# Optimization experiments

Measured on AMD Instinct MI355X. Metric: run time of the kernel, lower is better.

## Reference

```python
import jax, jax.numpy as jnp
import numpy as np

DIM = 384
HEADS = 8
SR = 2
BN_EPS = 1e-5


def setup_inputs() -> dict:
    key = jax.random.key(0)
    ks = jax.random.split(key, 8)
    B, Hh, Ww = 4, 64, 64
    N = Hh * Ww
    Nk = (Hh // SR) * (Ww // SR)
    w = lambda k, s: jax.random.normal(k, s, jnp.float32) * 0.02
    return {
        "x": jax.random.normal(ks[0], (B, N, DIM), jnp.float32),
        "relative_pos": jax.random.normal(ks[1], (HEADS, N, Nk), jnp.float32) * 0.02,
        "H": Hh,
        "W": Ww,
        "Wq": w(ks[2], (DIM, DIM)),
        "Wk": w(ks[3], (DIM, DIM)),
        "Wv": w(ks[4], (DIM, DIM)),
        "Wp": w(ks[5], (DIM, DIM)),
        "bp": jnp.zeros((DIM,), jnp.float32),
        "sr_w": w(ks[6], (DIM, 1, SR, SR)),  # depthwise conv, OIHW with groups=DIM
        "sr_b": jnp.zeros((DIM,), jnp.float32),
        "bn_gamma": jnp.ones((DIM,), jnp.float32),
        "bn_beta": jnp.zeros((DIM,), jnp.float32),
        "bn_mean": jnp.zeros((DIM,), jnp.float32),
        "bn_var": jnp.ones((DIM,), jnp.float32),
    }


def reference(x, relative_pos, Wq, Wk, Wv, Wp, bp, sr_w, sr_b,
              bn_gamma, bn_beta, bn_mean, bn_var, H, W):
    B, N, C = x.shape
    hd = C // HEADS
    scale = hd ** (-0.5)
    # q projection -> [B, heads, N, hd]
    q = (x @ Wq.T).reshape(B, N, HEADS, hd).transpose(0, 2, 1, 3)
    # spatial reduction: depthwise conv stride SR + BatchNorm (eval mode)
    x_ = x.transpose(0, 2, 1).reshape(B, C, H, W)
    y = jax.lax.conv_general_dilated(
        x_, sr_w, window_strides=(SR, SR), padding="VALID",
        feature_group_count=C,
        dimension_numbers=("NCHW", "OIHW", "NCHW"))
    y = y + sr_b[None, :, None, None]
    inv = jax.lax.rsqrt(bn_var + BN_EPS) * bn_gamma
    y = (y - bn_mean[None, :, None, None]) * inv[None, :, None, None] \
        + bn_beta[None, :, None, None]
    xk = y.reshape(B, C, -1).transpose(0, 2, 1)  # [B, Nk, C]
    Nk = xk.shape[1]
    k = (xk @ Wk.T).reshape(B, Nk, HEADS, hd).transpose(0, 2, 1, 3)
    v = (xk @ Wv.T).reshape(B, Nk, HEADS, hd).transpose(0, 2, 1, 3)
    # scores with additive relative-position bias (broadcast over batch)
    attn = jnp.einsum("bhnd,bhmd->bhnm", q, k) * scale + relative_pos
    attn = jax.nn.softmax(attn, axis=-1)
    out = jnp.einsum("bhnm,bhmd->bhnd", attn, v)
    out = out.transpose(0, 2, 1, 3).reshape(B, N, C)
    return out @ Wp.T + bp
```

## Files before the change

kernel.cpp:

```cpp
#include <hip/hip_runtime.h>
#include <hip/hip_bf16.h>

#define LOG2E 1.4426950408889634f

typedef short bf16x8 __attribute__((ext_vector_type(8)));
typedef float f32x4  __attribute__((ext_vector_type(4)));

#define OFF_BPf  16
#define OFF_SRWf (OFF_BPf + 384)
#define OFF_SRBf (OFF_SRWf + 1536)
#define OFF_GAf  (OFF_SRBf + 384)
#define OFF_BEf  (OFF_GAf + 384)
#define OFF_MUf  (OFF_BEf + 384)
#define OFF_VAf  (OFF_MUf + 384)
#define U_XB 7712
#define U_WQ (U_XB + 6291456)
#define U_WK (U_WQ + 147456)
#define U_WV (U_WK + 147456)
#define U_WP (U_WV + 147456)
#define U_XK (U_WP + 147456)
#define U_QB (U_XK + 1572864)
#define U_KB (U_QB + 6291456)
#define U_VT (U_KB + 1572864)
#define U_OB (U_VT + 1572864)

static __device__ __forceinline__ float bfu(unsigned short u){ return __uint_as_float(((unsigned)u) << 16); }
static __device__ __forceinline__ float bf_lo(unsigned v){ return __uint_as_float(v << 16); }
static __device__ __forceinline__ float bf_hi(unsigned v){ return __uint_as_float(v & 0xFFFF0000u); }
static __device__ __forceinline__ unsigned short f2bf(float f){
  unsigned u = __float_as_uint(f);
  u += 0x7FFFu + ((u >> 16) & 1u);
  return (unsigned short)(u >> 16);
}
static __device__ __forceinline__ unsigned pkcvt(float a, float b){
  float2 f; f.x = a; f.y = b;
  __hip_bfloat162 h = __float22bfloat162_rn(f);
  union { __hip_bfloat162 h2; unsigned u; } cv; cv.h2 = h; return cv.u;
}
static __device__ __forceinline__ unsigned pk2bf(float a, float b){
  return pkcvt(a, b);
}
static __device__ __forceinline__ float fast_exp2(float x){ return __builtin_amdgcn_exp2f(x); }
static __device__ __forceinline__ void gld_lds16(const void* g, void* l){
  __builtin_amdgcn_global_load_lds((const __attribute__((address_space(1))) void*)g,
                                   (__attribute__((address_space(3))) void*)l, 16, 0, 0);
}

__global__ void detect_bf16(const unsigned* __restrict__ xraw, int* __restrict__ flag){
  unsigned w = xraw[threadIdx.x];
  unsigned e = (w >> 7) & 0xFFu;
  unsigned long long m = __ballot(e >= 118u && e <= 137u);
  if (threadIdx.x == 0) *flag = (__popcll(m) >= 40) ? 1 : 0;
}

static __device__ __forceinline__ void cp8_bf(unsigned short* dst, const void* src, int off, bool bf){
  if (bf) { *(uint4*)dst = *(const uint4*)((const unsigned short*)src + off); }
  else {
    const float* s = (const float*)src + off;
    float4 a = *(const float4*)s, b = *(const float4*)(s + 4);
    uint4 o; o.x = pk2bf(a.x, a.y); o.y = pk2bf(a.z, a.w);
    o.z = pk2bf(b.x, b.y); o.w = pk2bf(b.z, b.w);
    *(uint4*)dst = o;
  }
}
static __device__ __forceinline__ void cp8_f(float* dst, const void* src, int off, bool bf){
  if (bf) {
    const unsigned short* s = (const unsigned short*)src + off;
    uint4 w = *(const uint4*)s;
    float4 a, b;
    a.x = bf_lo(w.x); a.y = bf_hi(w.x); a.z = bf_lo(w.y); a.w = bf_hi(w.y);
    b.x = bf_lo(w.z); b.y = bf_hi(w.z); b.z = bf_lo(w.w); b.w = bf_hi(w.w);
    *(float4*)dst = a; *(float4*)(dst + 4) = b;
  } else {
    const float* s = (const float*)src + off;
    *(float4*)dst = *(const float4*)s;
    *(float4*)(dst + 4) = *(const float4*)(s + 4);
  }
}

__global__ __launch_bounds__(256) void convert_all(
    const void* x, const void* wq, const void* wk, const void* wv, const void* wp,
    const void* bp, const void* srw, const void* srb, const void* ga, const void* be,
    const void* mu, const void* va, float* ws){
  const bool bf = ((const int*)ws)[0] != 0;
  unsigned short* u = (unsigned short*)ws;
  int g = blockIdx.x * 256 + threadIdx.x;
  if (g < 786432) { cp8_bf(u + U_XB + g*8, x,  g*8, bf); return; }  g -= 786432;
  if (g < 18432)  { cp8_bf(u + U_WQ + g*8, wq, g*8, bf); return; }  g -= 18432;
  if (g < 18432)  { cp8_bf(u + U_WK + g*8, wk, g*8, bf); return; }  g -= 18432;
  if (g < 18432)  { cp8_bf(u + U_WV + g*8, wv, g*8, bf); return; }  g -= 18432;
  if (g < 18432)  { cp8_bf(u + U_WP + g*8, wp, g*8, bf); return; }  g -= 18432;
  if (g < 192)    { cp8_f(ws + OFF_SRWf + g*8, srw, g*8, bf); return; } g -= 192;
  if (g < 48)     { cp8_f(ws + OFF_BPf  + g*8, bp,  g*8, bf); return; } g -= 48;
  if (g < 48)     { cp8_f(ws + OFF_SRBf + g*8, srb, g*8, bf); return; } g -= 48;
  if (g < 48)     { cp8_f(ws + OFF_GAf  + g*8, ga,  g*8, bf); return; } g -= 48;
  if (g < 48)     { cp8_f(ws + OFF_BEf  + g*8, be,  g*8, bf); return; } g -= 48;
  if (g < 48)     { cp8_f(ws + OFF_MUf  + g*8, mu,  g*8, bf); return; } g -= 48;
  if (g < 48)     { cp8_f(ws + OFF_VAf  + g*8, va,  g*8, bf); }
}

__global__ __launch_bounds__(256) void sr_bn(const unsigned short* __restrict__ xb,
    const float* __restrict__ wsf, unsigned short* __restrict__ xkb){
  int idx = blockIdx.x * 256 + threadIdx.x;
  int c8 = idx % 48;
  int nk = (idx / 48) & 1023;
  int b  = idx / (48 * 1024);
  int i = nk >> 5, j = nk & 31;
  int c0 = c8 * 8;
  const unsigned short* xp = xb + ((size_t)(b*4096 + i*128 + j*2))*384 + c0;
  unsigned aw[4], bw[4], cw[4], dw[4];
  *(uint4*)aw = *(const uint4*)(xp);
  *(uint4*)bw = *(const uint4*)(xp + 384);
  *(uint4*)cw = *(const uint4*)(xp + 64*384);
  *(uint4*)dw = *(const uint4*)(xp + 65*384);
  unsigned out[4];
  #pragma unroll
  for (int k2 = 0; k2 < 4; ++k2) {
    float r2[2];
    #pragma unroll
    for (int half = 0; half < 2; ++half) {
      int k = k2*2 + half;
      int c = c0 + k;
      float xa = half ? bf_hi(aw[k2]) : bf_lo(aw[k2]);
      float xbv = half ? bf_hi(bw[k2]) : bf_lo(bw[k2]);
      float xc = half ? bf_hi(cw[k2]) : bf_lo(cw[k2]);
      float xd = half ? bf_hi(dw[k2]) : bf_lo(dw[k2]);
      float acc = xa*wsf[OFF_SRWf+c*4] + xbv*wsf[OFF_SRWf+c*4+1]
                + xc*wsf[OFF_SRWf+c*4+2] + xd*wsf[OFF_SRWf+c*4+3];
      float inv = rsqrtf(wsf[OFF_VAf+c] + 1e-5f) * wsf[OFF_GAf+c];
      r2[half] = (acc + wsf[OFF_SRBf+c] - wsf[OFF_MUf+c]) * inv + wsf[OFF_BEf+c];
    }
    out[k2] = pkcvt(r2[0], r2[1]);
  }
  *(uint4*)(xkb + (size_t)idx*8) = *(uint4*)out;
}

__global__ __launch_bounds__(256) void proj_qkv(unsigned short* __restrict__ u){
  int z, by;
  if (blockIdx.y < 128)      { z = 0; by = blockIdx.y; }
  else if (blockIdx.y < 160) { z = 1; by = blockIdx.y - 128; }
  else                       { z = 2; by = blockIdx.y - 160; }
  const unsigned short* A = u + ((z == 0) ? U_XB : U_XK);
  const unsigned short* W = u + ((z == 0) ? U_WQ : (z == 1) ? U_WK : U_WV);

  __shared__ unsigned short As[128][40];
  __shared__ unsigned short Ws[128][40];
  const int tid = threadIdx.x;
  const int wave = tid >> 6, lane = tid & 63, lg = lane >> 4, ln = lane & 15;
  const int m0 = by * 128, n0 = blockIdx.x * 128;
  const int wm = (wave >> 1) * 64, wn = (wave & 1) * 64;
  f32x4 acc[4][4];
  #pragma unroll
  for (int i = 0; i < 4; ++i)
    #pragma unroll
    for (int j = 0; j < 4; ++j) acc[i][j] = (f32x4){0.f,0.f,0.f,0.f};

  const int arow = tid >> 1, acol = (tid & 1) * 16;
  for (int kt = 0; kt < 384; kt += 32) {
    uint4 a0 = *(const uint4*)&A[(size_t)(m0+arow)*384 + kt + acol];
    uint4 a1 = *(const uint4*)&A[(size_t)(m0+arow)*384 + kt + acol + 8];
    uint4 w0 = *(const uint4*)&W[(size_t)(n0+arow)*384 + kt + acol];
    uint4 w1 = *(const uint4*)&W[(size_t)(n0+arow)*384 + kt + acol + 8];
    __syncthreads();
    *(uint4*)&As[arow][acol] = a0;  *(uint4*)&As[arow][acol+8] = a1;
    *(uint4*)&Ws[arow][acol] = w0;  *(uint4*)&Ws[arow][acol+8] = w1;
    __syncthreads();
    bf16x8 af[4], wf[4];
    #pragma unroll
    for (int mi = 0; mi < 4; ++mi) af[mi] = *(const bf16x8*)&As[wm + mi*16 + ln][lg*8];
    #pragma unroll
    for (int ni = 0; ni < 4; ++ni) wf[ni] = *(const bf16x8*)&Ws[wn + ni*16 + ln][lg*8];
    #pragma unroll
    for (int mi = 0; mi < 4; ++mi)
      #pragma unroll
      for (int ni = 0; ni < 4; ++ni)
        acc[mi][ni] = __builtin_amdgcn_mfma_f32_16x16x32_bf16(af[mi], wf[ni], acc[mi][ni], 0, 0, 0);
  }

  unsigned short* outQ = u + U_QB;
  unsigned short* outK = u + U_KB;
  unsigned short* outV = u + U_VT;
  #pragma unroll
  for (int mi = 0; mi < 4; ++mi)
    #pragma unroll
    for (int ni = 0; ni < 4; ++ni) {
      int gcol = n0 + wn + ni*16 + ln;
      if (z == 2) {
        int grow0 = m0 + wm + mi*16 + lg*4;
        int hh = gcol / 48, d = gcol - hh*48;
        int bb = grow0 >> 10, mk = grow0 & 1023;
        uint2 st; st.x = pkcvt(acc[mi][ni][0], acc[mi][ni][1]);
        st.y = pkcvt(acc[mi][ni][2], acc[mi][ni][3]);
        *(uint2*)&outV[((size_t)((bb*8 + hh)*48 + d))*1024 + mk] = st;
      } else {
        unsigned short* dst = (z == 0) ? outQ : outK;
        #pragma unroll
        for (int r = 0; r < 4; ++r) {
          int grow = m0 + wm + mi*16 + lg*4 + r;
          dst[(size_t)grow*384 + gcol] = f2bf(acc[mi][ni][r]);
        }
      }
    }
}

__global__ __launch_bounds__(256) void gemm_out(const unsigned short* __restrict__ A,
    const unsigned short* __restrict__ W, const float* __restrict__ bias,
    void* __restrict__ out, const int* __restrict__ flag){
  __shared__ unsigned short As[128][40];
  __shared__ unsigned short Ws[128][40];
  const int tid = threadIdx.x;
  const int wave = tid >> 6, lane = tid & 63, lg = lane >> 4, ln = lane & 15;
  const int m0 = blockIdx.y * 128, n0 = blockIdx.x * 128;
  const int wm = (wave >> 1) * 64, wn = (wave & 1) * 64;
  f32x4 acc[4][4];
  #pragma unroll
  for (int i = 0; i < 4; ++i)
    #pragma unroll
    for (int j = 0; j < 4; ++j) acc[i][j] = (f32x4){0.f,0.f,0.f,0.f};

  const int arow = tid >> 1, acol = (tid & 1) * 16;
  for (int kt = 0; kt < 384; kt += 32) {
    uint4 a0 = *(const uint4*)&A[(size_t)(m0+arow)*384 + kt + acol];
    uint4 a1 = *(const uint4*)&A[(size_t)(m0+arow)*384 + kt + acol + 8];
    uint4 w0 = *(const uint4*)&W[(size_t)(n0+arow)*384 + kt + acol];
    uint4 w1 = *(const uint4*)&W[(size_t)(n0+arow)*384 + kt + acol + 8];
    __syncthreads();
    *(uint4*)&As[arow][acol] = a0;  *(uint4*)&As[arow][acol+8] = a1;
    *(uint4*)&Ws[arow][acol] = w0;  *(uint4*)&Ws[arow][acol+8] = w1;
    __syncthreads();
    bf16x8 af[4], wf[4];
    #pragma unroll
    for (int mi = 0; mi < 4; ++mi) af[mi] = *(const bf16x8*)&As[wm + mi*16 + ln][lg*8];
    #pragma unroll
    for (int ni = 0; ni < 4; ++ni) wf[ni] = *(const bf16x8*)&Ws[wn + ni*16 + ln][lg*8];
    #pragma unroll
    for (int mi = 0; mi < 4; ++mi)
      #pragma unroll
      for (int ni = 0; ni < 4; ++ni)
        acc[mi][ni] = __builtin_amdgcn_mfma_f32_16x16x32_bf16(af[mi], wf[ni], acc[mi][ni], 0, 0, 0);
  }

  const bool bff = (*flag != 0);
  #pragma unroll
  for (int mi = 0; mi < 4; ++mi)
    #pragma unroll
    for (int ni = 0; ni < 4; ++ni)
      #pragma unroll
      for (int r = 0; r < 4; ++r) {
        int grow = m0 + wm + mi*16 + lg*4 + r;
        int gcol = n0 + wn + ni*16 + ln;
        float v = acc[mi][ni][r] + bias[gcol];
        if (bff) ((unsigned short*)out)[(size_t)grow*384 + gcol] = f2bf(v);
        else     ((float*)out)[(size_t)grow*384 + gcol] = v;
      }
}

__global__ __launch_bounds__(256, 4) void attn_mfma(const unsigned short* __restrict__ qb,
    const unsigned short* __restrict__ kb, const unsigned short* __restrict__ vt,
    const void* __restrict__ rel, const int* __restrict__ flag,
    unsigned short* __restrict__ ob){
  __shared__ __align__(16) unsigned short Kbuf[2][6*512];
  __shared__ __align__(16) unsigned short Vbuf[8*384];
  __shared__ __align__(16) unsigned short Ps[4][16][64];
  __shared__ float Ls[4][32];
  const int x = blockIdx.x;
  const int b = x >> 5, nb = x & 31, h = blockIdx.y;
  const int tid = threadIdx.x, wave = tid >> 6, lane = tid & 63;
  const int lg = lane >> 4, ln = lane & 15;
  const int qrow0 = nb * 128 + wave * 32;
  const bool bfm = (*flag != 0);
  const float SCL = 0.14433756729740643f * LOG2E;

  bf16x8 qf0[2], qf1[2];
  #pragma unroll
  for (int qt = 0; qt < 2; ++qt) {
    const unsigned short* qp = qb + ((size_t)(b*4096 + qrow0 + qt*16 + ln))*384 + h*48;
    qf0[qt] = *(const bf16x8*)(qp + lg*8);
    bf16x8 z = {0,0,0,0,0,0,0,0};
    if (lg < 2) z = *(const bf16x8*)(qp + 32 + lg*8);
    qf1[qt] = z;
  }

  f32x4 o[2][3];
  #pragma unroll
  for (int qt = 0; qt < 2; ++qt) { o[qt][0] = (f32x4){0.f,0.f,0.f,0.f}; o[qt][1] = o[qt][0]; o[qt][2] = o[qt][0]; }
  float lsum[2] = {0.f, 0.f};

  const float* relf = (const float*)rel;
  const unsigned short* relh = (const unsigned short*)rel;
  const size_t rbase = ((size_t)(h*4096 + qrow0 + ln)) * 1024;
  const size_t kbase = (size_t)(b*1024) * 384 + (size_t)h*48;
  const size_t vbase = ((size_t)(b*8 + h)) * 48 * 1024;

  const unsigned swz = (unsigned)((ln & 7) << 4);
  char* psrow = (char*)&Ps[wave][ln][0];

  const int jk1 = wave;
  const int jk2 = 4 + wave;
  const int jv1 = wave;
  const int jv2 = 2 + wave;
  int s1i = jv1*64 + lane;  int c1 = s1i/48, d1 = s1i - 48*c1;
  size_t vg1 = vbase + (size_t)d1*1024 + c1*8;
  int s2i = jv2*64 + lane;  int c2 = s2i/48, d2 = s2i - 48*c2;
  size_t vg2 = vbase + (size_t)d2*1024 + c2*8;

  gld_lds16(kb + kbase + (size_t)lane*384 + jk1*8, &Kbuf[0][jk1*512]);
  if (wave < 2) gld_lds16(kb + kbase + (size_t)lane*384 + jk2*8, &Kbuf[0][jk2*512]);

  #pragma unroll 1
  for (int t = 0; t < 16; ++t) {
    const int cbuf = t & 1, nbuf = cbuf ^ 1;
    __syncthreads();

    uint2 rr[2][4];
    if (bfm) {
      #pragma unroll
      for (int qt = 0; qt < 2; ++qt)
        #pragma unroll
        for (int mt = 0; mt < 4; ++mt)
          rr[qt][mt] = *(const uint2*)(relh + rbase + (size_t)qt*16384 + t*64 + mt*16 + lg*4);
    } else {
      #pragma unroll
      for (int qt = 0; qt < 2; ++qt)
        #pragma unroll
        for (int mt = 0; mt < 4; ++mt) {
          float4 q_ = *(const float4*)(relf + rbase + (size_t)qt*16384 + t*64 + mt*16 + lg*4);
          rr[qt][mt].x = pkcvt(q_.x, q_.y); rr[qt][mt].y = pkcvt(q_.z, q_.w);
        }
    }

    gld_lds16(vt + vg1 + t*64, &Vbuf[jv1*512]);
    if (wave >= 2) gld_lds16(vt + vg2 + t*64, &Vbuf[jv2*512]);
    const int T = (t + 1 < 16) ? t + 1 : 15;
    gld_lds16(kb + kbase + (size_t)T*24576 + (size_t)lane*384 + jk1*8, &Kbuf[nbuf][jk1*512]);
    if (wave < 2) gld_lds16(kb + kbase + (size_t)T*24576 + (size_t)lane*384 + jk2*8, &Kbuf[nbuf][jk2*512]);

    f32x4 s0[4];
    #pragma unroll
    for (int mt = 0; mt < 4; ++mt) {
      bf16x8 k0 = *(const bf16x8*)&Kbuf[cbuf][lg*512 + (mt*16 + ln)*8];
      bf16x8 k1 = {0,0,0,0,0,0,0,0};
      if (lg < 2) k1 = *(const bf16x8*)&Kbuf[cbuf][(4 + lg)*512 + (mt*16 + ln)*8];
      s0[mt] = __builtin_amdgcn_mfma_f32_16x16x32_bf16(k0, qf0[0], (f32x4){0.f,0.f,0.f,0.f}, 0, 0, 0);
      s0[mt] = __builtin_amdgcn_mfma_f32_16x16x32_bf16(k1, qf1[0], s0[mt], 0, 0, 0);
    }
    {
      float lacc = 0.f;
      #pragma unroll
      for (int mt = 0; mt < 4; ++mt) {
        float r0 = bf_lo(rr[0][mt].x), r1 = bf_hi(rr[0][mt].x);
        float r2 = bf_lo(rr[0][mt].y), r3 = bf_hi(rr[0][mt].y);
        float p0 = fast_exp2(fmaf(s0[mt][0], SCL, r0 * LOG2E));
        float p1 = fast_exp2(fmaf(s0[mt][1], SCL, r1 * LOG2E));
        float p2 = fast_exp2(fmaf(s0[mt][2], SCL, r2 * LOG2E));
        float p3 = fast_exp2(fmaf(s0[mt][3], SCL, r3 * LOG2E));
        lacc += (p0 + p1) + (p2 + p3);
        uint2 w; w.x = pkcvt(p0, p1); w.y = pkcvt(p2, p3);
        *(uint2*)(psrow + (((unsigned)(mt*32 + lg*8)) ^ swz)) = w;
      }
      lsum[0] += lacc;
    }

    __syncthreads();

    #pragma unroll
    for (int ks = 0; ks < 2; ++ks) {
      bf16x8 vf[3];
      #pragma unroll
      for (int nd = 0; nd < 3; ++nd)
        vf[nd] = *(const bf16x8*)&Vbuf[(ks*4 + lg)*384 + (nd*16 + ln)*8];
      bf16x8 pa = *(const bf16x8*)(psrow + (((unsigned)(ks*64 + lg*16)) ^ swz));
      #pragma unroll
      for (int nd = 0; nd < 3; ++nd)
        o[0][nd] = __builtin_amdgcn_mfma_f32_16x16x32_bf16(pa, vf[nd], o[0][nd], 0, 0, 0);
    }

    f32x4 s1[4];
    #pragma unroll
    for (int mt = 0; mt < 4; ++mt) {
      bf16x8 k0 = *(const bf16x8*)&Kbuf[cbuf][lg*512 + (mt*16 + ln)*8];
      bf16x8 k1 = {0,0,0,0,0,0,0,0};
      if (lg < 2) k1 = *(const bf16x8*)&Kbuf[cbuf][(4 + lg)*512 + (mt*16 + ln)*8];
      s1[mt] = __builtin_amdgcn_mfma_f32_16x16x32_bf16(k0, qf0[1], (f32x4){0.f,0.f,0.f,0.f}, 0, 0, 0);
      s1[mt] = __builtin_amdgcn_mfma_f32_16x16x32_bf16(k1, qf1[1], s1[mt], 0, 0, 0);
    }
    {
      float lacc = 0.f;
      #pragma unroll
      for (int mt = 0; mt < 4; ++mt) {
        float r0 = bf_lo(rr[1][mt].x), r1 = bf_hi(rr[1][mt].x);
        float r2 = bf_lo(rr[1][mt].y), r3 = bf_hi(rr[1][mt].y);
        float p0 = fast_exp2(fmaf(s1[mt][0], SCL, r0 * LOG2E));
        float p1 = fast_exp2(fmaf(s1[mt][1], SCL, r1 * LOG2E));
        float p2 = fast_exp2(fmaf(s1[mt][2], SCL, r2 * LOG2E));
        float p3 = fast_exp2(fmaf(s1[mt][3], SCL, r3 * LOG2E));
        lacc += (p0 + p1) + (p2 + p3);
        uint2 w; w.x = pkcvt(p0, p1); w.y = pkcvt(p2, p3);
        *(uint2*)(psrow + (((unsigned)(mt*32 + lg*8)) ^ swz)) = w;
      }
      lsum[1] += lacc;
    }
    #pragma unroll
    for (int ks = 0; ks < 2; ++ks) {
      bf16x8 vf[3];
      #pragma unroll
      for (int nd = 0; nd < 3; ++nd)
        vf[nd] = *(const bf16x8*)&Vbuf[(ks*4 + lg)*384 + (nd*16 + ln)*8];
      bf16x8 pa = *(const bf16x8*)(psrow + (((unsigned)(ks*64 + lg*16)) ^ swz));
      #pragma unroll
      for (int nd = 0; nd < 3; ++nd)
        o[1][nd] = __builtin_amdgcn_mfma_f32_16x16x32_bf16(pa, vf[nd], o[1][nd], 0, 0, 0);
    }
  }

  #pragma unroll
  for (int qt = 0; qt < 2; ++qt) {
    lsum[qt] += __shfl_xor(lsum[qt], 16, 64);
    lsum[qt] += __shfl_xor(lsum[qt], 32, 64);
    if (lg == 0) Ls[wave][qt*16 + ln] = lsum[qt];
  }
  #pragma unroll
  for (int qt = 0; qt < 2; ++qt)
    #pragma unroll
    for (int r = 0; r < 4; ++r) {
      float l = Ls[wave][qt*16 + lg*4 + r];
      float linv = 1.0f / l;
      size_t rowb = ((size_t)(b*4096 + qrow0 + qt*16 + lg*4 + r))*384 + h*48 + ln;
      #pragma unroll
      for (int nd = 0; nd < 3; ++nd)
        ob[rowb + nd*16] = f2bf(o[qt][nd][r] * linv);
    }
}

extern "C" void kernel_launch(void* const* d_in, const int* in_sizes, int n_in,
                              void* d_out, int out_size, void* d_ws, size_t ws_size,
                              hipStream_t stream) {
  float* ws = (float*)d_ws;
  int* flag = (int*)d_ws;
  unsigned short* u = (unsigned short*)d_ws;

  detect_bf16<<<1, 64, 0, stream>>>((const unsigned*)d_in[0], flag);
  convert_all<<<3363, 256, 0, stream>>>(d_in[0], d_in[4], d_in[5], d_in[6], d_in[7],
      d_in[8], d_in[9], d_in[10], d_in[11], d_in[12], d_in[13], d_in[14], ws);
  sr_bn<<<768, 256, 0, stream>>>(u + U_XB, ws, u + U_XK);
  proj_qkv<<<dim3(3, 192), 256, 0, stream>>>(u);
  attn_mfma<<<dim3(128, 8), 256, 0, stream>>>(u + U_QB, u + U_KB, u + U_VT, d_in[1], flag, u + U_OB);
  gemm_out<<<dim3(3, 128), 256, 0, stream>>>(u + U_OB, u + U_WP, ws + OFF_BPf, d_out, flag);
}
```

Measured before the change: 356.3 us.

## Split attention key range in two with a separate combine kernel

The attention kernel now splits the 16 key tiles into two halves on a doubled grid. Each half writes unnormalized bf16 partial outputs and per-row exp sums to workspace, and a new combine kernel adds the halves and normalizes. The aim is more parallelism and shorter per-block serial loops. The cost is an extra kernel launch, extra global traffic for the partials, and extra bf16 rounding of unnormalized partial sums.

```diff
diff --git a/kernel.cpp b/kernel.cpp
--- a/kernel.cpp
+++ b/kernel.cpp
@@ -23,6 +23,8 @@
 #define U_KB (U_QB + 6291456)
 #define U_VT (U_KB + 1572864)
 #define U_OB (U_VT + 1572864)
+#define U_PO1 (U_OB + 6291456)
+#define U_PL  (U_PO1 + 6291456)
 
 static __device__ __forceinline__ float bfu(unsigned short u){ return __uint_as_float(((unsigned)u) << 16); }
 static __device__ __forceinline__ float bf_lo(unsigned v){ return __uint_as_float(v << 16); }
@@ -258,13 +260,14 @@
 __global__ __launch_bounds__(256, 4) void attn_mfma(const unsigned short* __restrict__ qb,
     const unsigned short* __restrict__ kb, const unsigned short* __restrict__ vt,
     const void* __restrict__ rel, const int* __restrict__ flag,
-    unsigned short* __restrict__ ob){
+    unsigned short* __restrict__ ob, float* __restrict__ pl){
   __shared__ __align__(16) unsigned short Kbuf[2][6*512];
   __shared__ __align__(16) unsigned short Vbuf[8*384];
   __shared__ __align__(16) unsigned short Ps[4][16][64];
-  __shared__ float Ls[4][32];
   const int x = blockIdx.x;
-  const int b = x >> 5, nb = x & 31, h = blockIdx.y;
+  const int b = x >> 5, nb = x & 31;
+  const int h = blockIdx.y & 7, sp = blockIdx.y >> 3;
+  const int t0 = sp * 8, t1 = t0 + 8;
   const int tid = threadIdx.x, wave = tid >> 6, lane = tid & 63;
   const int lg = lane >> 4, ln = lane & 15;
   const int qrow0 = nb * 128 + wave * 32;
@@ -304,11 +307,11 @@
   int s2i = jv2*64 + lane;  int c2 = s2i/48, d2 = s2i - 48*c2;
   size_t vg2 = vbase + (size_t)d2*1024 + c2*8;
 
-  gld_lds16(kb + kbase + (size_t)lane*384 + jk1*8, &Kbuf[0][jk1*512]);
-  if (wave < 2) gld_lds16(kb + kbase + (size_t)lane*384 + jk2*8, &Kbuf[0][jk2*512]);
+  gld_lds16(kb + kbase + (size_t)t0*24576 + (size_t)lane*384 + jk1*8, &Kbuf[0][jk1*512]);
+  if (wave < 2) gld_lds16(kb + kbase + (size_t)t0*24576 + (size_t)lane*384 + jk2*8, &Kbuf[0][jk2*512]);
 
   #pragma unroll 1
-  for (int t = 0; t < 16; ++t) {
+  for (int t = t0; t < t1; ++t) {
     const int cbuf = t & 1, nbuf = cbuf ^ 1;
     __syncthreads();
 
@@ -331,7 +334,7 @@
 
     gld_lds16(vt + vg1 + t*64, &Vbuf[jv1*512]);
     if (wave >= 2) gld_lds16(vt + vg2 + t*64, &Vbuf[jv2*512]);
-    const int T = (t + 1 < 16) ? t + 1 : 15;
+    const int T = (t + 1 < t1) ? t + 1 : t;
     gld_lds16(kb + kbase + (size_t)T*24576 + (size_t)lane*384 + jk1*8, &Kbuf[nbuf][jk1*512]);
     if (wave < 2) gld_lds16(kb + kbase + (size_t)T*24576 + (size_t)lane*384 + jk2*8, &Kbuf[nbuf][jk2*512]);
 
@@ -413,23 +416,45 @@
     }
   }
 
+  unsigned short* po = ob + (size_t)sp * 6291456;
   #pragma unroll
   for (int qt = 0; qt < 2; ++qt) {
     lsum[qt] += __shfl_xor(lsum[qt], 16, 64);
     lsum[qt] += __shfl_xor(lsum[qt], 32, 64);
-    if (lg == 0) Ls[wave][qt*16 + ln] = lsum[qt];
+    if (lg == 0)
+      pl[(size_t)sp*131072 + (size_t)(b*8 + h)*4096 + qrow0 + qt*16 + ln] = lsum[qt];
   }
   #pragma unroll
   for (int qt = 0; qt < 2; ++qt)
     #pragma unroll
     for (int r = 0; r < 4; ++r) {
-      float l = Ls[wave][qt*16 + lg*4 + r];
-      float linv = 1.0f / l;
       size_t rowb = ((size_t)(b*4096 + qrow0 + qt*16 + lg*4 + r))*384 + h*48 + ln;
       #pragma unroll
       for (int nd = 0; nd < 3; ++nd)
-        ob[rowb + nd*16] = f2bf(o[qt][nd][r] * linv);
-    }
+        po[rowb + nd*16] = f2bf(o[qt][nd][r]);
+    }
+}
+
+__global__ __launch_bounds__(256) void attn_combine(unsigned short* __restrict__ ob,
+    const float* __restrict__ pl){
+  int idx = blockIdx.x * 256 + threadIdx.x;
+  int c8 = idx % 48;
+  int n  = (idx / 48) & 4095;
+  int b  = idx / (48 * 4096);
+  int c0 = c8 * 8;
+  int h  = c8 / 6;
+  size_t base = ((size_t)(b*4096 + n))*384 + c0;
+  uint4 a = *(const uint4*)(ob + base);
+  uint4 c = *(const uint4*)(ob + 6291456 + base);
+  float l0 = pl[(size_t)(b*8 + h)*4096 + n];
+  float l1 = pl[131072 + (size_t)(b*8 + h)*4096 + n];
+  float inv = 1.0f / (l0 + l1);
+  unsigned w[4];
+  w[0] = pkcvt((bf_lo(a.x)+bf_lo(c.x))*inv, (bf_hi(a.x)+bf_hi(c.x))*inv);
+  w[1] = pkcvt((bf_lo(a.y)+bf_lo(c.y))*inv, (bf_hi(a.y)+bf_hi(c.y))*inv);
+  w[2] = pkcvt((bf_lo(a.z)+bf_lo(c.z))*inv, (bf_hi(a.z)+bf_hi(c.z))*inv);
+  w[3] = pkcvt((bf_lo(a.w)+bf_lo(c.w))*inv, (bf_hi(a.w)+bf_hi(c.w))*inv);
+  *(uint4*)(ob + base) = *(uint4*)w;
 }
 
 extern "C" void kernel_launch(void* const* d_in, const int* in_sizes, int n_in,
@@ -444,6 +469,8 @@
       d_in[8], d_in[9], d_in[10], d_in[11], d_in[12], d_in[13], d_in[14], ws);
   sr_bn<<<768, 256, 0, stream>>>(u + U_XB, ws, u + U_XK);
   proj_qkv<<<dim3(3, 192), 256, 0, stream>>>(u);
-  attn_mfma<<<dim3(128, 8), 256, 0, stream>>>(u + U_QB, u + U_KB, u + U_VT, d_in[1], flag, u + U_OB);
+  attn_mfma<<<dim3(128, 16), 256, 0, stream>>>(u + U_QB, u + U_KB, u + U_VT, d_in[1], flag,
+      u + U_OB, (float*)(u + U_PL));
+  attn_combine<<<3072, 256, 0, stream>>>(u + U_OB, (const float*)(u + U_PL));
   gemm_out<<<dim3(3, 128), 256, 0, stream>>>(u + U_OB, u + U_WP, ws + OFF_BPf, d_out, flag);
 }
```

After: 369.0 us. +3.6%, slower.
